# Kernel tuning notes

Hardware: AMD Instinct MI355X
Metric: run time of the kernel (lower is better)

Reference implementation:

```python
import jax, jax.numpy as jnp
import numpy as np

KY = KX = 3  # kernel_size
PAD_Y = (KY - 1) // 2
PAD_X = (KX - 1) // 2


def setup_inputs() -> dict:
    key = jax.random.key(0)
    x = jax.random.uniform(key, (8, 3, 512, 512), dtype=jnp.float32)
    return {"x": x}


def reference(x) -> jnp.ndarray:
    # Median blur: zero-pad, gather the KYxKX neighborhood per pixel,
    # take the (lower) median along the window axis, matching
    # torch's conv2d(one-hot)+median(dim=2)[0].
    b, c, h, w = x.shape
    xp = jnp.pad(x, ((0, 0), (0, 0), (PAD_Y, PAD_Y), (PAD_X, PAD_X)))
    # (B, C, KY*KX, H, W) -- same intermediate layout as the torch im2col
    patches = jnp.stack(
        [xp[:, :, i:i + h, j:j + w] for i in range(KY) for j in range(KX)],
        axis=2,
    )
    n = KY * KX
    s = jnp.sort(patches, axis=2)
    # torch.median returns the lower median (index (n-1)//2 of sorted values)
    return s[:, :, (n - 1) // 2]
```

## Files before the change

### kernel.cpp

```cpp
#include <hip/hip_runtime.h>


#define MB_W 512
#define MB_H 512
#define MB_PLANES (8 * 3)
#define MB_ROWS (MB_PLANES * MB_H)
#define MB_THREADS (MB_ROWS * (MB_W / 4))

__device__ __forceinline__ float median9(float p0, float p1, float p2,
                                         float p3, float p4, float p5,
                                         float p6, float p7, float p8) {
#define CE(a, b) { float t_ = fminf(a, b); b = fmaxf(a, b); a = t_; }
    CE(p1, p2); CE(p4, p5); CE(p7, p8);
    CE(p0, p1); CE(p3, p4); CE(p6, p7);
    CE(p1, p2); CE(p4, p5); CE(p7, p8);
    CE(p0, p3); CE(p5, p8); CE(p4, p7);
    CE(p3, p6); CE(p1, p4); CE(p2, p5);
    CE(p4, p7); CE(p4, p2); CE(p6, p4);
    CE(p4, p2);
#undef CE
    return p4;
}

__global__ __launch_bounds__(256) void median_blur_kernel(
        const float* __restrict__ in, float* __restrict__ out) {
    const int gid = blockIdx.x * blockDim.x + threadIdx.x;
    const int xq = gid & 127;
    const int r  = gid >> 7;
    const int y  = r & (MB_H - 1);
    const int x0 = xq << 2;

    const float* rowc = in + (size_t)r * MB_W;

    float a[3][6];
    #pragma unroll
    for (int dy = 0; dy < 3; ++dy) {
        const int yy = y + dy - 1;
        const float* rp = rowc + (ptrdiff_t)(dy - 1) * MB_W;
        if (yy >= 0 && yy < MB_H) {
            const float4 v = *reinterpret_cast<const float4*>(rp + x0);
            a[dy][1] = v.x; a[dy][2] = v.y; a[dy][3] = v.z; a[dy][4] = v.w;
            a[dy][0] = (x0 > 0)       ? rp[x0 - 1] : 0.0f;
            a[dy][5] = (x0 + 4 < MB_W) ? rp[x0 + 4] : 0.0f;
        } else {
            #pragma unroll
            for (int k = 0; k < 6; ++k) a[dy][k] = 0.0f;
        }
    }

    float res[4];
    #pragma unroll
    for (int j = 0; j < 4; ++j) {
        res[j] = median9(a[0][j], a[0][j + 1], a[0][j + 2],
                         a[1][j], a[1][j + 1], a[1][j + 2],
                         a[2][j], a[2][j + 1], a[2][j + 2]);
    }

    float4 o;
    o.x = res[0]; o.y = res[1]; o.z = res[2]; o.w = res[3];
    *reinterpret_cast<float4*>(out + (size_t)r * MB_W + x0) = o;
}

extern "C" void kernel_launch(void* const* d_in, const int* in_sizes, int n_in,
                              void* d_out, int out_size, void* d_ws, size_t ws_size,
                              hipStream_t stream) {
    const float* x = (const float*)d_in[0];
    float* out = (float*)d_out;
    const int threads = 256;
    const int blocks = MB_THREADS / threads;
    median_blur_kernel<<<blocks, threads, 0, stream>>>(x, out);
}
```

Baseline: 80.27 us.

## Replace 19-exchange median network with column-sorted med3 median-of-9 scheme

Sorts each of the six input columns once using min3/med3/max3, shares those sorted columns across the four outputs, and takes each median as med3(max of lows, med of mids, min of highs) using the hardware fmed3 instruction. This cuts the ALU work per pixel compared with a full 19-exchange network per output. The kernel is largely memory bound, so the arithmetic savings may not show up in time. NaN handling of fmed3 may differ from the fmin/fmax network.

Measured after the change: 79.86 us. No clear change (-0.5%).

```diff
diff --git a/kernel.cpp b/kernel.cpp
--- a/kernel.cpp
+++ b/kernel.cpp
@@ -7,19 +7,14 @@
 #define MB_ROWS (MB_PLANES * MB_H)
 #define MB_THREADS (MB_ROWS * (MB_W / 4))
 
-__device__ __forceinline__ float median9(float p0, float p1, float p2,
-                                         float p3, float p4, float p5,
-                                         float p6, float p7, float p8) {
-#define CE(a, b) { float t_ = fminf(a, b); b = fmaxf(a, b); a = t_; }
-    CE(p1, p2); CE(p4, p5); CE(p7, p8);
-    CE(p0, p1); CE(p3, p4); CE(p6, p7);
-    CE(p1, p2); CE(p4, p5); CE(p7, p8);
-    CE(p0, p3); CE(p5, p8); CE(p4, p7);
-    CE(p3, p6); CE(p1, p4); CE(p2, p5);
-    CE(p4, p7); CE(p4, p2); CE(p6, p4);
-    CE(p4, p2);
-#undef CE
-    return p4;
+__device__ __forceinline__ float min3f(float a, float b, float c) {
+    return fminf(fminf(a, b), c);
+}
+__device__ __forceinline__ float max3f(float a, float b, float c) {
+    return fmaxf(fmaxf(a, b), c);
+}
+__device__ __forceinline__ float med3f(float a, float b, float c) {
+    return __builtin_amdgcn_fmed3f(a, b, c);
 }
 
 __global__ __launch_bounds__(256) void median_blur_kernel(
@@ -32,28 +27,50 @@
 
     const float* rowc = in + (size_t)r * MB_W;
 
-    float a[3][6];
+    float a0[6], a1[6], a2[6];
+
+    {
+        const float4 v = *reinterpret_cast<const float4*>(rowc + x0);
+        a1[1] = v.x; a1[2] = v.y; a1[3] = v.z; a1[4] = v.w;
+        a1[0] = (x0 > 0)        ? rowc[x0 - 1] : 0.0f;
+        a1[5] = (x0 + 4 < MB_W) ? rowc[x0 + 4] : 0.0f;
+    }
+    if (y > 0) {
+        const float* rp = rowc - MB_W;
+        const float4 v = *reinterpret_cast<const float4*>(rp + x0);
+        a0[1] = v.x; a0[2] = v.y; a0[3] = v.z; a0[4] = v.w;
+        a0[0] = (x0 > 0)        ? rp[x0 - 1] : 0.0f;
+        a0[5] = (x0 + 4 < MB_W) ? rp[x0 + 4] : 0.0f;
+    } else {
+        #pragma unroll
+        for (int k = 0; k < 6; ++k) a0[k] = 0.0f;
+    }
+    if (y < MB_H - 1) {
+        const float* rp = rowc + MB_W;
+        const float4 v = *reinterpret_cast<const float4*>(rp + x0);
+        a2[1] = v.x; a2[2] = v.y; a2[3] = v.z; a2[4] = v.w;
+        a2[0] = (x0 > 0)        ? rp[x0 - 1] : 0.0f;
+        a2[5] = (x0 + 4 < MB_W) ? rp[x0 + 4] : 0.0f;
+    } else {
+        #pragma unroll
+        for (int k = 0; k < 6; ++k) a2[k] = 0.0f;
+    }
+
+    float lo[6], mi[6], hi[6];
     #pragma unroll
-    for (int dy = 0; dy < 3; ++dy) {
-        const int yy = y + dy - 1;
-        const float* rp = rowc + (ptrdiff_t)(dy - 1) * MB_W;
-        if (yy >= 0 && yy < MB_H) {
-            const float4 v = *reinterpret_cast<const float4*>(rp + x0);
-            a[dy][1] = v.x; a[dy][2] = v.y; a[dy][3] = v.z; a[dy][4] = v.w;
-            a[dy][0] = (x0 > 0)       ? rp[x0 - 1] : 0.0f;
-            a[dy][5] = (x0 + 4 < MB_W) ? rp[x0 + 4] : 0.0f;
-        } else {
-            #pragma unroll
-            for (int k = 0; k < 6; ++k) a[dy][k] = 0.0f;
-        }
+    for (int k = 0; k < 6; ++k) {
+        lo[k] = min3f(a0[k], a1[k], a2[k]);
+        mi[k] = med3f(a0[k], a1[k], a2[k]);
+        hi[k] = max3f(a0[k], a1[k], a2[k]);
     }
 
     float res[4];
     #pragma unroll
     for (int j = 0; j < 4; ++j) {
-        res[j] = median9(a[0][j], a[0][j + 1], a[0][j + 2],
-                         a[1][j], a[1][j + 1], a[1][j + 2],
-                         a[2][j], a[2][j + 1], a[2][j + 2]);
+        const float A = max3f(lo[j], lo[j + 1], lo[j + 2]);
+        const float B = med3f(mi[j], mi[j + 1], mi[j + 2]);
+        const float C = min3f(hi[j], hi[j + 1], hi[j + 2]);
+        res[j] = med3f(A, B, C);
     }
 
     float4 o;
```
